# Performance work log

Measured on AMD Instinct MI355X. Metric: run time of the kernel, lower is better.

The kernel has to match this reference:

```python
import jax, jax.numpy as jnp
import numpy as np
from jax import lax

B, CIN, H, W = 16, 128, 56, 56
COUT, K, STRIDE, PAD, DIL = 256, 3, 1, 1, 1
D = 8  # lattice.d
KE = K * K
M = CIN * KE // D  # sub-vectors per spatial position


def setup_inputs() -> dict:
    key = jax.random.key(0)
    k1, k2, k3 = jax.random.split(key, 3)
    input_encodings = jax.random.normal(k1, (B, CIN, H, W), dtype=jnp.float32)
    weight_encodings = jax.random.normal(k2, (COUT, M, D), dtype=jnp.float32)
    bias = jax.random.normal(k3, (COUT,), dtype=jnp.float32)
    return {"input_encodings": input_encodings,
            "weight_encodings": weight_encodings,
            "bias": bias}


def reference(input_encodings, weight_encodings, bias):
    b, cin, h, w = input_encodings.shape
    cout, m, d = weight_encodings.shape
    h_out = (h + 2 * PAD - DIL * (K - 1) - 1) // STRIDE + 1
    w_out = (w + 2 * PAD - DIL * (K - 1) - 1) // STRIDE + 1
    L = h_out * w_out
    # im2col / unfold: (B, Cin*K*K, Hout, Wout), channel-major (c, kh, kw) ordering
    patches = lax.conv_general_dilated_patches(
        input_encodings, (K, K), (STRIDE, STRIDE), [(PAD, PAD), (PAD, PAD)],
        rhs_dilation=(DIL, DIL))
    # (B, L, M, D): each position split into M lattice-encoded sub-vectors of dim D
    x = patches.reshape(b, cin * K * K, L).transpose(0, 2, 1).reshape(b, L, m, d)
    # two-sided vLUT matrix multiply == sum of per-sub-vector inner products
    out = jnp.einsum('blmd,omd->bol', x, weight_encodings)  # (B, Cout, L)
    out = out.reshape(b, cout, h_out, w_out)
    return out + bias[None, :, None, None]
```

## Files before the change

kernel.cpp:

```cpp
#include <hip/hip_runtime.h>
#include <hip/hip_bf16.h>

#define CIN_   128
#define HW_    56
#define LHW_   3136
#define COUT_  256
#define KTOT_  1152
#define TH_    2
#define SPT_   112
#define NF_    7
#define SCOLS_ 58
#define SPP_   232
#define CSTR_  128

typedef unsigned short u16;
typedef __attribute__((ext_vector_type(8))) short short8v;
typedef __attribute__((ext_vector_type(4))) float f32x4;

__device__ __forceinline__ u16 f2bf(float f) {
  union { float f; unsigned u; } v; v.f = f;
  unsigned u = v.u;
  u += 0x7fffu + ((u >> 16) & 1u);
  return (u16)(u >> 16);
}
__device__ __forceinline__ unsigned pack2(u16 a, u16 b) {
  return (unsigned)a | ((unsigned)b << 16);
}

__global__ void wreorder_kernel(const float* __restrict__ w, u16* __restrict__ wb) {
  int j = blockIdx.x * 256 + threadIdx.x;
  int c4 = j & 31;
  int o  = (j >> 5) & 255;
  int t  = j >> 13;
  const float* src = w + (size_t)o * KTOT_ + t;
  ushort4 r;
  r.x = f2bf(src[(c4 * 4 + 0) * 9]);
  r.y = f2bf(src[(c4 * 4 + 1) * 9]);
  r.z = f2bf(src[(c4 * 4 + 2) * 9]);
  r.w = f2bf(src[(c4 * 4 + 3) * 9]);
  *reinterpret_cast<ushort4*>(wb + ((size_t)(t * 256 + o) * CSTR_ + c4 * 4)) = r;
}

__global__ __launch_bounds__(256, 2) void conv2_kernel(
    const float* __restrict__ in, const u16* __restrict__ wb,
    const float* __restrict__ bias, float* __restrict__ out)
{
  __shared__ u16 xs[SPP_ * CSTR_];

  const int tid  = threadIdx.x;
  const int lane = tid & 63;
  const int wid  = tid >> 6;
  const int lr   = lane & 15;
  const int lg   = lane >> 4;

  const int bid = blockIdx.x;
  const int ch  = bid & 1;
  const int ty  = (bid >> 1) % 28;
  const int b   = bid / 56;

  const float* inb = in + (size_t)b * CIN_ * LHW_;
  const int iy0 = ty * TH_ - 1;

  #pragma unroll 1
  for (int i = 0; i < 15; ++i) {
    int idx = i * 256 + tid;
    if (idx < SPP_ * 16) {
      int cg  = idx / SPP_;
      int spp = idx - cg * SPP_;
      int rr  = spp / SCOLS_;
      int cc  = spp - rr * SCOLS_;
      int iy  = iy0 + rr;
      int ix  = cc - 1;
      bool ok = ((unsigned)iy < (unsigned)HW_) && ((unsigned)ix < (unsigned)HW_);
      const float* p = inb + (size_t)cg * 8 * LHW_ + iy * HW_ + ix;
      u16 v[8];
      #pragma unroll
      for (int jj = 0; jj < 8; ++jj)
        v[jj] = f2bf(ok ? p[jj * LHW_] : 0.f);
      uint4 pk;
      pk.x = pack2(v[0], v[1]); pk.y = pack2(v[2], v[3]);
      pk.z = pack2(v[4], v[5]); pk.w = pack2(v[6], v[7]);
      *reinterpret_cast<uint4*>(&xs[spp * CSTR_ + ((cg * 8) ^ ((spp & 7) << 3))]) = pk;
    }
  }

  int spp0[NF_];
  #pragma unroll
  for (int nf = 0; nf < NF_; ++nf) {
    int sp = nf * 16 + lr;
    int r  = (sp >= 56) ? 1 : 0;
    int x  = sp - r * 56;
    spp0[nf] = (r + 1) * SCOLS_ + x + 1;
  }

  f32x4 acc[2][NF_];
  #pragma unroll
  for (int m = 0; m < 2; ++m)
    #pragma unroll
    for (int nf = 0; nf < NF_; ++nf)
      acc[m][nf] = f32x4{0.f, 0.f, 0.f, 0.f};

  __syncthreads();

  const u16* wt0 = wb + (size_t)(ch * 128 + wid * 32 + lr) * CSTR_ + lg * 8;

  #pragma unroll 1
  for (int t = 0; t < 9; ++t) {
    const int dspp = (t / 3 - 1) * SCOLS_ + (t % 3 - 1);
    const u16* wt = wt0 + (size_t)t * 256 * CSTR_;
    #pragma unroll
    for (int c0i = 0; c0i < 4; ++c0i) {
      const int c0 = c0i * 32;
      short8v a0 = *reinterpret_cast<const short8v*>(wt + c0);
      short8v a1 = *reinterpret_cast<const short8v*>(wt + 16 * CSTR_ + c0);
      short8v bv[NF_];
      #pragma unroll
      for (int nf = 0; nf < NF_; ++nf) {
        int spp = spp0[nf] + dspp;
        int off = spp * CSTR_ + ((c0 + lg * 8) ^ ((spp & 7) << 3));
        bv[nf] = *reinterpret_cast<const short8v*>(&xs[off]);
      }
      #pragma unroll
      for (int nf = 0; nf < NF_; ++nf) {
        acc[0][nf] = __builtin_amdgcn_mfma_f32_16x16x32_bf16(a0, bv[nf], acc[0][nf], 0, 0, 0);
        acc[1][nf] = __builtin_amdgcn_mfma_f32_16x16x32_bf16(a1, bv[nf], acc[1][nf], 0, 0, 0);
      }
    }
  }

  float* ob = out + (size_t)b * COUT_ * LHW_ + ty * SPT_;
  const int obase = ch * 128 + wid * 32 + lg * 4;
  #pragma unroll
  for (int m = 0; m < 2; ++m) {
    #pragma unroll
    for (int rr = 0; rr < 4; ++rr) {
      const int o = obase + m * 16 + rr;
      const float bs = bias[o];
      #pragma unroll
      for (int nf = 0; nf < NF_; ++nf)
        ob[(size_t)o * LHW_ + nf * 16 + lr] = acc[m][nf][rr] + bs;
    }
  }
}

#define SPT0_  64
#define BK0_   32
#define NKS0_  36
#define LDSW0_ 40

__global__ __launch_bounds__(256, 2) void conv_fb_kernel(
    const float* __restrict__ in, const float* __restrict__ wf,
    const float* __restrict__ bias, float* __restrict__ out)
{
  __shared__ u16 xs[SPT0_ * LDSW0_];
  const int tid = threadIdx.x;
  const int lane = tid & 63;
  const int wid = tid >> 6;
  const int lg = lane >> 4;
  const int lr = lane & 15;
  const int bid = blockIdx.x;
  const int b = bid / 49;
  const int l0 = (bid % 49) * SPT0_;
  const int sp = tid & 63;
  const int qq = tid >> 6;
  const int l = l0 + sp;
  const int y = l / HW_;
  const int x = l - y * HW_;
  const float* inb = in + (size_t)b * CIN_ * LHW_;

  f32x4 acc[4][4];
  #pragma unroll
  for (int i = 0; i < 4; ++i)
    #pragma unroll
    for (int j = 0; j < 4; ++j) acc[i][j] = f32x4{0.f, 0.f, 0.f, 0.f};

  auto stage_load = [&](int ks) -> uint4 {
    int kbase = ks * BK0_ + qq * 8;
    int c = kbase / 9;
    int t = kbase - c * 9;
    u16 v[8];
    #pragma unroll
    for (int j = 0; j < 8; ++j) {
      int dy = (t * 11) >> 5;
      int dx = t - 3 * dy;
      int yy = y + dy - 1, xx = x + dx - 1;
      float f = 0.f;
      if ((unsigned)yy < (unsigned)HW_ && (unsigned)xx < (unsigned)HW_)
        f = inb[(c * HW_ + yy) * HW_ + xx];
      v[j] = f2bf(f);
      ++t; if (t == 9) { t = 0; ++c; }
    }
    uint4 r;
    r.x = pack2(v[0], v[1]); r.y = pack2(v[2], v[3]);
    r.z = pack2(v[4], v[5]); r.w = pack2(v[6], v[7]);
    return r;
  };

  uint4 st = stage_load(0);
  for (int ks = 0; ks < NKS0_; ++ks) {
    __syncthreads();
    *reinterpret_cast<uint4*>(&xs[sp * LDSW0_ + qq * 8]) = st;
    __syncthreads();
    if (ks + 1 < NKS0_) st = stage_load(ks + 1);
    const int k0 = ks * BK0_;
    short8v a[4];
    #pragma unroll
    for (int ai = 0; ai < 4; ++ai) {
      const int o = wid * 64 + ai * 16 + lr;
      const float* p = wf + (size_t)o * KTOT_ + k0 + lg * 8;
      u16 t8[8];
      #pragma unroll
      for (int j = 0; j < 8; ++j) t8[j] = f2bf(p[j]);
      union { uint4 u; short8v s; } cv;
      cv.u.x = pack2(t8[0], t8[1]); cv.u.y = pack2(t8[2], t8[3]);
      cv.u.z = pack2(t8[4], t8[5]); cv.u.w = pack2(t8[6], t8[7]);
      a[ai] = cv.s;
    }
    short8v bv[4];
    #pragma unroll
    for (int sj = 0; sj < 4; ++sj)
      bv[sj] = *reinterpret_cast<const short8v*>(&xs[(sj * 16 + lr) * LDSW0_ + lg * 8]);
    #pragma unroll
    for (int ai = 0; ai < 4; ++ai)
      #pragma unroll
      for (int sj = 0; sj < 4; ++sj)
        acc[ai][sj] = __builtin_amdgcn_mfma_f32_16x16x32_bf16(a[ai], bv[sj], acc[ai][sj], 0, 0, 0);
  }
  float* outb = out + (size_t)b * COUT_ * LHW_ + l0;
  #pragma unroll
  for (int ai = 0; ai < 4; ++ai)
    #pragma unroll
    for (int r = 0; r < 4; ++r) {
      const int o = wid * 64 + ai * 16 + lg * 4 + r;
      const float bvs = bias[o];
      #pragma unroll
      for (int sj = 0; sj < 4; ++sj)
        outb[(size_t)o * LHW_ + sj * 16 + lr] = acc[ai][sj][r] + bvs;
    }
}

extern "C" void kernel_launch(void* const* d_in, const int* in_sizes, int n_in,
                              void* d_out, int out_size, void* d_ws, size_t ws_size,
                              hipStream_t stream) {
  (void)in_sizes; (void)n_in; (void)out_size;
  const float* in   = (const float*)d_in[0];
  const float* w    = (const float*)d_in[1];
  const float* bias = (const float*)d_in[2];
  float* out = (float*)d_out;

  const size_t wbytes = (size_t)COUT_ * KTOT_ * sizeof(u16);
  if (ws_size >= wbytes) {
    u16* wb = (u16*)d_ws;
    wreorder_kernel<<<dim3(288), dim3(256), 0, stream>>>(w, wb);
    conv2_kernel<<<dim3(896), dim3(256), 0, stream>>>(in, wb, bias, out);
  } else {
    conv_fb_kernel<<<dim3(784), dim3(256), 0, stream>>>(in, w, bias, out);
  }
}
```

Before: 71.05 us.

## Pre-convert input to NHWC bf16 and stage halo tiles via direct global-to-LDS loads

Adds a pre-pass that transposes the fp32 NCHW input into an NHWC bf16 buffer in the workspace. A new conv kernel with 512 threads per block covers all 256 output channels per block and fills its swizzled LDS halo tile with global_load_lds 16-byte copies, using a zero page for padding. Blocks are remapped with a swizzle. The aim is to replace the strided fp32 gathers and per-element conversions in the staging phase with coalesced async copies, and to stop loading each input tile twice for the two channel halves. The cost is one extra kernel launch plus an extra global round trip of the converted input, and the workspace requirement grows.

```diff
diff --git a/kernel.cpp b/kernel.cpp
--- a/kernel.cpp
+++ b/kernel.cpp
@@ -27,7 +27,12 @@
   return (unsigned)a | ((unsigned)b << 16);
 }
 
-__global__ void wreorder_kernel(const float* __restrict__ w, u16* __restrict__ wb) {
+__global__ void wreorder_kernel(const float* __restrict__ w, u16* __restrict__ wb,
+                                u16* __restrict__ zp) {
+  if (zp && blockIdx.x == 0 && threadIdx.x < 16) {
+    uint4 z; z.x = z.y = z.z = z.w = 0u;
+    reinterpret_cast<uint4*>(zp)[threadIdx.x] = z;
+  }
   int j = blockIdx.x * 256 + threadIdx.x;
   int c4 = j & 31;
   int o  = (j >> 5) & 255;
@@ -41,23 +46,153 @@
   *reinterpret_cast<ushort4*>(wb + ((size_t)(t * 256 + o) * CSTR_ + c4 * 4)) = r;
 }
 
+#define TLDSW_ 136
+__global__ __launch_bounds__(256) void nhwc_kernel(
+    const float* __restrict__ in, u16* __restrict__ xin) {
+  __shared__ u16 ts[64 * TLDSW_];
+  const int bp = blockIdx.x;
+  const int b = bp / 49;
+  const int pos0 = (bp % 49) * 64;
+  const int tid = threadIdx.x;
+  const float* ib = in + (size_t)b * CIN_ * LHW_ + pos0;
+  {
+    const int p  = tid & 63;
+    const int c0 = (tid >> 6) * 32;
+    #pragma unroll
+    for (int i = 0; i < 32; ++i)
+      ts[p * TLDSW_ + c0 + i] = f2bf(ib[(size_t)(c0 + i) * LHW_ + p]);
+  }
+  __syncthreads();
+  {
+    const int p  = tid >> 2;
+    const int c0 = (tid & 3) * 32;
+    u16* dst = xin + ((size_t)b * LHW_ + pos0 + p) * CIN_ + c0;
+    const u16* srcr = &ts[p * TLDSW_ + c0];
+    #pragma unroll
+    for (int j = 0; j < 4; ++j)
+      reinterpret_cast<uint4*>(dst)[j] =
+          *reinterpret_cast<const uint4*>(srcr + j * 8);
+  }
+}
+
+__device__ __forceinline__ void gload_lds16(const void* g, void* l) {
+  __builtin_amdgcn_global_load_lds(
+      (const __attribute__((address_space(1))) void*)g,
+      (__attribute__((address_space(3))) void*)l, 16, 0, 0);
+}
+
+__global__ __launch_bounds__(512, 4) void conv3_kernel(
+    const u16* __restrict__ xin, const u16* __restrict__ wb,
+    const float* __restrict__ bias, const u16* __restrict__ zpage,
+    float* __restrict__ out)
+{
+  __shared__ u16 xs[SPP_ * CSTR_];
+
+  const int tid  = threadIdx.x;
+  const int lane = tid & 63;
+  const int wid  = tid >> 6;
+  const int lr   = lane & 15;
+  const int lg   = lane >> 4;
+
+  const int swz = (blockIdx.x & 7) * 56 + (blockIdx.x >> 3);
+  const int b   = swz / 28;
+  const int ty  = swz % 28;
+  const int iy0 = ty * TH_ - 1;
+
+  const u16* xb = xin + (size_t)b * LHW_ * CIN_;
+
+  auto stage_one = [&](int idx) {
+    int spp   = idx >> 4;
+    int chunk = idx & 15;
+    int rr = spp / SCOLS_;
+    int cc = spp - rr * SCOLS_;
+    int iy = iy0 + rr;
+    int ix = cc - 1;
+    int sch = chunk ^ (spp & 7);
+    const u16* src =
+        ((unsigned)iy < (unsigned)HW_ && (unsigned)ix < (unsigned)HW_)
+            ? xb + ((size_t)(iy * HW_ + ix) * CIN_ + sch * 8)
+            : zpage;
+    u16* ldst = xs + (size_t)(idx & ~63) * 8;
+    gload_lds16(src, ldst);
+  };
+  #pragma unroll
+  for (int i = 0; i < 7; ++i) stage_one(i * 512 + tid);
+  if (tid < 128) stage_one(3584 + tid);
+
+  int spp0[NF_];
+  #pragma unroll
+  for (int nf = 0; nf < NF_; ++nf) {
+    int sp = nf * 16 + lr;
+    int r  = (sp >= 56) ? 1 : 0;
+    int x  = sp - r * 56;
+    spp0[nf] = (r + 1) * SCOLS_ + (x + 1);
+  }
+
+  f32x4 acc[2][NF_];
+  #pragma unroll
+  for (int m = 0; m < 2; ++m)
+    #pragma unroll
+    for (int nf = 0; nf < NF_; ++nf)
+      acc[m][nf] = f32x4{0.f, 0.f, 0.f, 0.f};
+
+  __syncthreads();
+
+  const u16* wt0 = wb + (size_t)(wid * 32 + lr) * CSTR_ + lg * 8;
+
+  #pragma unroll
+  for (int t = 0; t < 9; ++t) {
+    const int dspp = (t / 3 - 1) * SCOLS_ + (t % 3 - 1);
+    const u16* wt = wt0 + (size_t)t * COUT_ * CSTR_;
+    #pragma unroll
+    for (int c0i = 0; c0i < 4; ++c0i) {
+      const int c0 = c0i * 32;
+      short8v a0 = *reinterpret_cast<const short8v*>(wt + c0);
+      short8v a1 = *reinterpret_cast<const short8v*>(wt + 16 * CSTR_ + c0);
+      short8v bv[NF_];
+      #pragma unroll
+      for (int nf = 0; nf < NF_; ++nf) {
+        int spp = spp0[nf] + dspp;
+        int off = (spp << 7) + ((c0 + lg * 8) ^ ((spp & 7) << 3));
+        bv[nf] = *reinterpret_cast<const short8v*>(&xs[off]);
+      }
+      #pragma unroll
+      for (int nf = 0; nf < NF_; ++nf) {
+        acc[0][nf] = __builtin_amdgcn_mfma_f32_16x16x32_bf16(a0, bv[nf], acc[0][nf], 0, 0, 0);
+        acc[1][nf] = __builtin_amdgcn_mfma_f32_16x16x32_bf16(a1, bv[nf], acc[1][nf], 0, 0, 0);
+      }
+    }
+  }
+
+  float* ob = out + (size_t)b * COUT_ * LHW_ + ty * SPT_;
+  const int obase = wid * 32 + lg * 4;
+  #pragma unroll
+  for (int m = 0; m < 2; ++m) {
+    #pragma unroll
+    for (int rr = 0; rr < 4; ++rr) {
+      const int o = obase + m * 16 + rr;
+      const float bs = bias[o];
+      #pragma unroll
+      for (int nf = 0; nf < NF_; ++nf)
+        ob[(size_t)o * LHW_ + nf * 16 + lr] = acc[m][nf][rr] + bs;
+    }
+  }
+}
+
 __global__ __launch_bounds__(256, 2) void conv2_kernel(
     const float* __restrict__ in, const u16* __restrict__ wb,
     const float* __restrict__ bias, float* __restrict__ out)
 {
   __shared__ u16 xs[SPP_ * CSTR_];
-
   const int tid  = threadIdx.x;
   const int lane = tid & 63;
   const int wid  = tid >> 6;
   const int lr   = lane & 15;
   const int lg   = lane >> 4;
-
   const int bid = blockIdx.x;
   const int ch  = bid & 1;
   const int ty  = (bid >> 1) % 28;
   const int b   = bid / 56;
-
   const float* inb = in + (size_t)b * CIN_ * LHW_;
   const int iy0 = ty * TH_ - 1;
 
@@ -83,7 +218,6 @@
       *reinterpret_cast<uint4*>(&xs[spp * CSTR_ + ((cg * 8) ^ ((spp & 7) << 3))]) = pk;
     }
   }
-
   int spp0[NF_];
   #pragma unroll
   for (int nf = 0; nf < NF_; ++nf) {
@@ -92,18 +226,14 @@
     int x  = sp - r * 56;
     spp0[nf] = (r + 1) * SCOLS_ + x + 1;
   }
-
   f32x4 acc[2][NF_];
   #pragma unroll
   for (int m = 0; m < 2; ++m)
     #pragma unroll
     for (int nf = 0; nf < NF_; ++nf)
       acc[m][nf] = f32x4{0.f, 0.f, 0.f, 0.f};
-
   __syncthreads();
-
   const u16* wt0 = wb + (size_t)(ch * 128 + wid * 32 + lr) * CSTR_ + lg * 8;
-
   #pragma unroll 1
   for (int t = 0; t < 9; ++t) {
     const int dspp = (t / 3 - 1) * SCOLS_ + (t % 3 - 1);
@@ -127,11 +257,10 @@
       }
     }
   }
-
   float* ob = out + (size_t)b * COUT_ * LHW_ + ty * SPT_;
   const int obase = ch * 128 + wid * 32 + lg * 4;
   #pragma unroll
-  for (int m = 0; m < 2; ++m) {
+  for (int m = 0; m < 2; ++m)
     #pragma unroll
     for (int rr = 0; rr < 4; ++rr) {
       const int o = obase + m * 16 + rr;
@@ -140,14 +269,12 @@
       for (int nf = 0; nf < NF_; ++nf)
         ob[(size_t)o * LHW_ + nf * 16 + lr] = acc[m][nf][rr] + bs;
     }
-  }
 }
 
 #define SPT0_  64
 #define BK0_   32
 #define NKS0_  36
 #define LDSW0_ 40
-
 __global__ __launch_bounds__(256, 2) void conv_fb_kernel(
     const float* __restrict__ in, const float* __restrict__ wf,
     const float* __restrict__ bias, float* __restrict__ out)
@@ -167,13 +294,11 @@
   const int y = l / HW_;
   const int x = l - y * HW_;
   const float* inb = in + (size_t)b * CIN_ * LHW_;
-
   f32x4 acc[4][4];
   #pragma unroll
   for (int i = 0; i < 4; ++i)
     #pragma unroll
     for (int j = 0; j < 4; ++j) acc[i][j] = f32x4{0.f, 0.f, 0.f, 0.f};
-
   auto stage_load = [&](int ks) -> uint4 {
     int kbase = ks * BK0_ + qq * 8;
     int c = kbase / 9;
@@ -195,7 +320,6 @@
     r.z = pack2(v[4], v[5]); r.w = pack2(v[6], v[7]);
     return r;
   };
-
   uint4 st = stage_load(0);
   for (int ks = 0; ks < NKS0_; ++ks) {
     __syncthreads();
@@ -248,10 +372,20 @@
   const float* bias = (const float*)d_in[2];
   float* out = (float*)d_out;
 
-  const size_t wbytes = (size_t)COUT_ * KTOT_ * sizeof(u16);
-  if (ws_size >= wbytes) {
+  const size_t wbytes  = (size_t)COUT_ * KTOT_ * sizeof(u16);
+  const size_t xbytes  = (size_t)16 * LHW_ * CIN_ * sizeof(u16);
+  const size_t need    = wbytes + xbytes + 256;
+
+  if (ws_size >= need) {
+    u16* wb  = (u16*)d_ws;
+    u16* xin = wb + wbytes / 2;
+    u16* zp  = xin + xbytes / 2;
+    wreorder_kernel<<<dim3(288), dim3(256), 0, stream>>>(w, wb, zp);
+    nhwc_kernel<<<dim3(784), dim3(256), 0, stream>>>(in, xin);
+    conv3_kernel<<<dim3(448), dim3(512), 0, stream>>>(xin, wb, bias, zp, out);
+  } else if (ws_size >= wbytes) {
     u16* wb = (u16*)d_ws;
-    wreorder_kernel<<<dim3(288), dim3(256), 0, stream>>>(w, wb);
+    wreorder_kernel<<<dim3(288), dim3(256), 0, stream>>>(w, wb, nullptr);
     conv2_kernel<<<dim3(896), dim3(256), 0, stream>>>(in, wb, bias, out);
   } else {
     conv_fb_kernel<<<dim3(784), dim3(256), 0, stream>>>(in, w, bias, out);
```

New measurement: 64.50 us. 1.1x faster.
